# Optimization experiments

Hardware: AMD Instinct MI355X
Metric: run time of the kernel (lower is better)

## Reference

```python
import jax, jax.numpy as jnp
import numpy as np

NEG = -1e30  # finite stand-in for -inf so softmax grads stay clean


def setup_inputs() -> dict:
    key = jax.random.key(0)
    k1, k2 = jax.random.split(key)
    C, D = 8192, 512
    gt_class_embeddings = jax.random.normal(k1, (C, D), dtype=jnp.float32)
    w = jax.random.normal(k2, (C, D), dtype=jnp.float32)
    return {"gt_class_embeddings": gt_class_embeddings, "w": w}


def reference(gt_class_embeddings, w):
    # L2-normalize class embeddings, cosine-similarity matrix S (diag == 1)
    G = gt_class_embeddings / jnp.linalg.norm(gt_class_embeddings, axis=-1, keepdims=True)
    S = G @ G.T  # [C, C]
    C = S.shape[0]
    off_diag = ~jnp.eye(C, dtype=bool)

    # seSoftmax: per-row softmax over entries != 1 (off-diagonal); diagonal stays 1
    P = jax.nn.softmax(jnp.where(off_diag, S, NEG), axis=-1)
    S2 = jnp.where(off_diag, P, 1.0)

    # argsort(-S2)[1] == most similar (diag value 1 always ranks first),
    # argsort(-S2)[-1] == least similar == row min (softmax values < 1)
    ms = jnp.argmax(jnp.where(off_diag, S2, NEG), axis=-1)  # [C]
    ls = jnp.argmin(jnp.where(off_diag, S2, -NEG), axis=-1)  # [C]

    rows = jnp.arange(C)
    margin = S2[rows, ms] - S2[rows, ls]  # [C]

    d_ms = jnp.sqrt(jnp.sum((w - w[ms]) ** 2, axis=-1))  # [C]
    d_ls = jnp.sqrt(jnp.sum((w - w[ls]) ** 2, axis=-1))  # [C]

    loss = jnp.mean(jnp.maximum(0.0, d_ms - d_ls + margin))
    return loss
```

## Files before the change

### kernel.cpp

```cpp
#include <hip/hip_runtime.h>
#include <math.h>

#define CDIM 8192
#define DDIM 512
#define NEGF -3.0e38f
#define POSF  3.0e38f

#define NSLOT 64

typedef __attribute__((ext_vector_type(8))) short bf16x8;
typedef __attribute__((ext_vector_type(4))) float f32x4;

__device__ __forceinline__ unsigned short f2bf(float x) {
    unsigned int u = __float_as_uint(x);
    u += 0x7fffu + ((u >> 16) & 1u);
    return (unsigned short)(u >> 16);
}
__device__ __forceinline__ float bf2f(unsigned short h) {
    return __uint_as_float(((unsigned int)h) << 16);
}
__device__ __forceinline__ void gld16(const void* g, void* l) {
    __builtin_amdgcn_global_load_lds(
        (__attribute__((address_space(1))) void*)(void*)g,
        (__attribute__((address_space(3))) void*)l, 16, 0, 0);
}

__global__ __launch_bounds__(256) void k_prep(const float* __restrict__ g,
                                              unsigned short* __restrict__ hi,
                                              unsigned short* __restrict__ lo) {
    const int wave = threadIdx.x >> 6;
    const int lane = threadIdx.x & 63;
    const int row = blockIdx.x * 4 + wave;
    const float4* src = (const float4*)(g + (size_t)row * DDIM);
    const float4 a = src[lane * 2];
    const float4 b = src[lane * 2 + 1];
    float s = a.x * a.x + a.y * a.y + a.z * a.z + a.w * a.w +
              b.x * b.x + b.y * b.y + b.z * b.z + b.w * b.w;
#pragma unroll
    for (int m = 1; m < 64; m <<= 1) s += __shfl_xor(s, m, 64);
    const float rn = rsqrtf(s);
    const float y[8] = {a.x * rn, a.y * rn, a.z * rn, a.w * rn,
                        b.x * rn, b.y * rn, b.z * rn, b.w * rn};
    unsigned int hv[4], lv[4];
#pragma unroll
    for (int i = 0; i < 4; ++i) {
        const unsigned short h0 = f2bf(y[2 * i]);
        const unsigned short h1 = f2bf(y[2 * i + 1]);
        const unsigned short l0 = f2bf(y[2 * i] - bf2f(h0));
        const unsigned short l1 = f2bf(y[2 * i + 1] - bf2f(h1));
        hv[i] = (unsigned int)h0 | ((unsigned int)h1 << 16);
        lv[i] = (unsigned int)l0 | ((unsigned int)l1 << 16);
    }
    uint4* dh = (uint4*)(hi + (size_t)row * DDIM + lane * 8);
    uint4* dl = (uint4*)(lo + (size_t)row * DDIM + lane * 8);
    *dh = make_uint4(hv[0], hv[1], hv[2], hv[3]);
    *dl = make_uint4(lv[0], lv[1], lv[2], lv[3]);
}

__global__ __launch_bounds__(512, 2) void k_simstats(
    const unsigned short* __restrict__ ghi, const unsigned short* __restrict__ glo,
    float* __restrict__ pmax, float* __restrict__ pmin, float* __restrict__ pZ,
    int* __restrict__ pamax, int* __restrict__ pamin) {
    const int bid = blockIdx.x;
    const int e = (bid & 7) * 132 + (bid >> 3);
    int J = 0, base = 0;
    while (true) {
        const int cnt = (J >> 1) + 1;
        if (e < base + cnt) break;
        base += cnt; ++J;
    }
    const int I = e - base;
    const bool typeD0 = (J == 2 * I);
    const bool typeD1 = (J == 2 * I + 1);

    __shared__ unsigned short SH[3 * 24576];
    const int t = threadIdx.x;
    const int wave = t >> 6;
    const int lane = t & 63;
    const int lanelo = lane & 15;
    const int quad = lane >> 4;
    const int wr = wave >> 1;
    const int wc = wave & 1;

    const int srow = t >> 2;
    const int scolb = ((t & 3) ^ ((t >> 3) & 3)) << 4;

    const int fsl = (quad ^ ((lanelo >> 1) & 3)) << 3;
    const int aoff = (wr * 64 + lanelo) * 32 + fsl;
    const int boff = (wc * 64 + lanelo) * 32 + fsl;

    float* rm  = (float*)SH;
    float* rmn = rm + 512;
    float* rz  = rmn + 512;
    int*   ra  = (int*)(rz + 512);
    int*   ran = ra + 512;
    float* cm  = (float*)(ran + 512);
    float* cmn = cm + 512;
    float* cz  = cmn + 512;
    int*   ca  = (int*)(cz + 512);
    int*   can = ca + 512;

    const int i0 = I * 256;
    const int j0 = J * 128;

    f32x4 acc[4][4];
#pragma unroll
    for (int rt = 0; rt < 4; ++rt)
#pragma unroll
        for (int ct = 0; ct < 4; ++ct)
            acc[rt][ct] = (f32x4){0.f, 0.f, 0.f, 0.f};

    const char* baseAh = (const char*)ghi + (size_t)(i0 + srow) * 1024 + scolb;
    const char* baseAl = (const char*)glo + (size_t)(i0 + srow) * 1024 + scolb;
    const char* baseBh = (const char*)ghi + (size_t)(j0 + srow) * 1024 + scolb;
    const char* baseBl = (const char*)glo + (size_t)(j0 + srow) * 1024 + scolb;

    auto STG_A = [&](int ks, int b, int half) {
        char* d = (char*)SH + b * 49152 + half * 16384 + t * 16;
        const char* gb = half ? baseAl : baseAh;
        const size_t cb = (size_t)ks * 64;
        gld16(gb + cb, d);
        gld16(gb + 131072 + cb, d + 8192);
    };
    auto STG_B = [&](int ks, int b, int half) {
        char* d = (char*)SH + b * 49152 + 32768 + half * 8192 + t * 16;
        const char* gb = half ? baseBl : baseBh;
        gld16(gb + (size_t)ks * 64, d);
    };

    STG_A(0, 0, 0); STG_A(0, 0, 1); STG_B(0, 0, 0); STG_B(0, 0, 1);
    STG_A(1, 1, 0); STG_A(1, 1, 1); STG_B(1, 1, 0); STG_B(1, 1, 1);
    asm volatile("s_waitcnt vmcnt(6)" ::: "memory");
    __builtin_amdgcn_s_barrier();
    asm volatile("" ::: "memory");

#pragma unroll
    for (int ks = 0; ks < 16; ++ks) {
        const unsigned short* buf = SH + (ks % 3) * 24576;
        const int sb = (ks + 2) % 3;
        const bool st = (ks <= 13);
        bf16x8 ah[4], bh[4];
        {
            if (st) STG_A(ks + 2, sb, 0);
            bf16x8 bl[4];
#pragma unroll
            for (int rt = 0; rt < 4; ++rt)
                ah[rt] = *(const bf16x8*)&buf[aoff + rt * 512];
#pragma unroll
            for (int ct = 0; ct < 4; ++ct)
                bl[ct] = *(const bf16x8*)&buf[20480 + boff + ct * 512];
            asm volatile("" ::: "memory");
            __builtin_amdgcn_s_barrier();
            asm volatile("s_waitcnt lgkmcnt(0)" ::: "memory");
            __builtin_amdgcn_s_setprio(1);
#pragma unroll
            for (int ct = 0; ct < 4; ++ct)
#pragma unroll
                for (int rt = 0; rt < 4; ++rt)
                    acc[rt][ct] = __builtin_amdgcn_mfma_f32_16x16x32_bf16(
                        ah[rt], bl[ct], acc[rt][ct], 0, 0, 0);
            __builtin_amdgcn_s_setprio(0);
            asm volatile("" ::: "memory");
            __builtin_amdgcn_s_barrier();
            asm volatile("" ::: "memory");
        }
        {
            if (st) STG_A(ks + 2, sb, 1);
#pragma unroll
            for (int ct = 0; ct < 4; ++ct)
                bh[ct] = *(const bf16x8*)&buf[16384 + boff + ct * 512];
            asm volatile("" ::: "memory");
            __builtin_amdgcn_s_barrier();
            asm volatile("s_waitcnt lgkmcnt(0)" ::: "memory");
            __builtin_amdgcn_s_setprio(1);
#pragma unroll
            for (int ct = 0; ct < 4; ++ct)
#pragma unroll
                for (int rt = 0; rt < 4; ++rt)
                    acc[rt][ct] = __builtin_amdgcn_mfma_f32_16x16x32_bf16(
                        ah[rt], bh[ct], acc[rt][ct], 0, 0, 0);
            __builtin_amdgcn_s_setprio(0);
            asm volatile("" ::: "memory");
            __builtin_amdgcn_s_barrier();
            asm volatile("" ::: "memory");
        }
        {
            if (st) { STG_B(ks + 2, sb, 0); STG_B(ks + 2, sb, 1); }
            bf16x8 al[4];
#pragma unroll
            for (int rt = 0; rt < 4; ++rt)
                al[rt] = *(const bf16x8*)&buf[8192 + aoff + rt * 512];
            if (ks <= 13) asm volatile("s_waitcnt vmcnt(6)" ::: "memory");
            else if (ks == 14) asm volatile("s_waitcnt vmcnt(0)" ::: "memory");
            asm volatile("" ::: "memory");
            __builtin_amdgcn_s_barrier();
            asm volatile("s_waitcnt lgkmcnt(0)" ::: "memory");
            __builtin_amdgcn_s_setprio(1);
#pragma unroll
            for (int ct = 0; ct < 4; ++ct)
#pragma unroll
                for (int rt = 0; rt < 4; ++rt)
                    acc[rt][ct] = __builtin_amdgcn_mfma_f32_16x16x32_bf16(
                        al[rt], bh[ct], acc[rt][ct], 0, 0, 0);
            __builtin_amdgcn_s_setprio(0);
            asm volatile("" ::: "memory");
            __builtin_amdgcn_s_barrier();
            asm volatile("" ::: "memory");
        }
    }

    const bool mask_d = (typeD0 && wr < 2) || (typeD1 && wr >= 2);

#pragma unroll
    for (int rt = 0; rt < 4; ++rt) {
#pragma unroll
        for (int r = 0; r < 4; ++r) {
            const int lrow = wr * 64 + rt * 16 + quad * 4 + r;
            const int gi = i0 + lrow;
            float tmax = NEGF; int targ = 0;
            float tmin = POSF; int targn = 0;
#pragma unroll
            for (int ct = 0; ct < 4; ++ct) {
                const int gj = j0 + wc * 64 + ct * 16 + lanelo;
                const float v = acc[rt][ct][r];
                const bool dg = mask_d && (gj == gi);
                const float vM = dg ? NEGF : v;
                const float vm = dg ? POSF : v;
                if (vM > tmax) { tmax = vM; targ = gj; }
                if (vm < tmin) { tmin = vm; targn = gj; }
            }
#pragma unroll
            for (int msk = 1; msk < 16; msk <<= 1) {
                const float v2 = __shfl_xor(tmax, msk, 64);
                const int i2 = __shfl_xor(targ, msk, 64);
                if (v2 > tmax) { tmax = v2; targ = i2; }
                const float v3 = __shfl_xor(tmin, msk, 64);
                const int i3 = __shfl_xor(targn, msk, 64);
                if (v3 < tmin) { tmin = v3; targn = i3; }
            }
            if (lanelo == 0) {
                const int o = wc * 256 + lrow;
                rm[o] = tmax; rmn[o] = tmin;
                ra[o] = targ; ran[o] = targn;
            }
        }
    }

    const bool col_ok = (!typeD0 && !typeD1) || (typeD1 && wr < 2);
    if (col_ok) {
#pragma unroll
        for (int ct = 0; ct < 4; ++ct) {
            const int lcol = wc * 64 + ct * 16 + lanelo;
            float tmax = NEGF; int targ = 0;
            float tmin = POSF; int targn = 0;
#pragma unroll
            for (int rt = 0; rt < 4; ++rt)
#pragma unroll
                for (int r = 0; r < 4; ++r) {
                    const int gi = i0 + wr * 64 + rt * 16 + quad * 4 + r;
                    const float v = acc[rt][ct][r];
                    if (v > tmax) { tmax = v; targ = gi; }
                    if (v < tmin) { tmin = v; targn = gi; }
                }
#pragma unroll
            for (int msk = 16; msk < 64; msk <<= 1) {
                const float m2v = __shfl_xor(tmax, msk, 64);
                const int i2 = __shfl_xor(targ, msk, 64);
                if (m2v > tmax) { tmax = m2v; targ = i2; }
                const float mn2 = __shfl_xor(tmin, msk, 64);
                const int in2 = __shfl_xor(targn, msk, 64);
                if (mn2 < tmin) { tmin = mn2; targn = in2; }
            }
            if (quad == 0) {
                const int o = wr * 128 + lcol;
                cm[o] = tmax; cmn[o] = tmin;
                ca[o] = targ; can[o] = targn;
            }
        }
    }

#pragma unroll
    for (int rt = 0; rt < 4; ++rt)
#pragma unroll
        for (int ct = 0; ct < 4; ++ct)
#pragma unroll
            for (int r = 0; r < 4; ++r)
                acc[rt][ct][r] = __expf(acc[rt][ct][r] - 1.f);
    if ((typeD0 && wr < 2 && wr == wc) ||
        (typeD1 && wr >= 2 && (wr - 2) == wc)) {
#pragma unroll
        for (int rt = 0; rt < 4; ++rt)
#pragma unroll
            for (int r = 0; r < 4; ++r)
                if (lanelo == quad * 4 + r) acc[rt][rt][r] = 0.f;
    }

#pragma unroll
    for (int rt = 0; rt < 4; ++rt)
#pragma unroll
        for (int r = 0; r < 4; ++r) {
            float s = acc[rt][0][r] + acc[rt][1][r] +
                      acc[rt][2][r] + acc[rt][3][r];
#pragma unroll
            for (int msk = 1; msk < 16; msk <<= 1) s += __shfl_xor(s, msk, 64);
            if (lanelo == 0)
                rz[wc * 256 + wr * 64 + rt * 16 + quad * 4 + r] = s;
        }

    if (col_ok) {
#pragma unroll
        for (int ct = 0; ct < 4; ++ct) {
            float s = 0.f;
#pragma unroll
            for (int rt = 0; rt < 4; ++rt)
                s += acc[rt][ct][0] + acc[rt][ct][1] +
                     acc[rt][ct][2] + acc[rt][ct][3];
#pragma unroll
            for (int msk = 16; msk < 64; msk <<= 1) s += __shfl_xor(s, msk, 64);
            if (quad == 0)
                cz[wr * 128 + wc * 64 + ct * 16 + lanelo] = s;
        }
    }

    __syncthreads();

    if (t < 256) {
        if (!(typeD0 && t >= 128)) {
            const float m0 = rm[t], m1 = rm[256 + t];
            float vmax = m0; int imax = ra[t];
            if (m1 > vmax) { vmax = m1; imax = ra[256 + t]; }
            float vmin = rmn[t]; int imin = ran[t];
            if (rmn[256 + t] < vmin) { vmin = rmn[256 + t]; imin = ran[256 + t]; }
            const size_t o = (size_t)J * CDIM + i0 + t;
            pmax[o] = vmax; pmin[o] = vmin; pZ[o] = rz[t] + rz[256 + t];
            pamax[o] = imax; pamin[o] = imin;
        }
    } else {
        const int tt = t - 256;
        const int h = tt >> 7;
        const int col = tt & 127;
        const bool ok = (!typeD0 && !typeD1) || (typeD1 && h == 0);
        if (ok) {
            const int b0 = h * 256 + col, b1 = h * 256 + 128 + col;
            const float m0 = cm[b0], m1 = cm[b1];
            float vmax = m0; int imax = ca[b0];
            if (m1 > vmax) { vmax = m1; imax = ca[b1]; }
            float vmin = cmn[b0]; int imin = can[b0];
            if (cmn[b1] < vmin) { vmin = cmn[b1]; imin = can[b1]; }
            const size_t o = (size_t)(2 * I + h) * CDIM + j0 + col;
            pmax[o] = vmax; pmin[o] = vmin; pZ[o] = cz[b0] + cz[b1];
            pamax[o] = imax; pamin[o] = imin;
        }
    }
}

__global__ __launch_bounds__(256) void k_lossc(
    const float* __restrict__ pmax, const float* __restrict__ pmin,
    const float* __restrict__ pZ, const int* __restrict__ pamax,
    const int* __restrict__ pamin, const float* __restrict__ w,
    float* __restrict__ vals) {
    const int wave = threadIdx.x >> 6;
    const int lane = threadIdx.x & 63;
    const int row = blockIdx.x * 4 + wave;
    const size_t o = (size_t)lane * CDIM + row;
    float v = pmax[o]; int a = pamax[o];
    float u = pmin[o]; int b = pamin[o];
    float z = pZ[o];
#pragma unroll
    for (int msk = 1; msk < 64; msk <<= 1) {
        const float v2 = __shfl_xor(v, msk, 64);
        const int i2 = __shfl_xor(a, msk, 64);
        if (v2 > v) { v = v2; a = i2; }
        const float v3 = __shfl_xor(u, msk, 64);
        const int i3 = __shfl_xor(b, msk, 64);
        if (v3 < u) { u = v3; b = i3; }
        z += __shfl_xor(z, msk, 64);
    }
    const float margin = (1.f - __expf(u - v)) * __expf(v - 1.f) / z;
    const int jm = a, jl = b;

    const float4* wi = (const float4*)(w + (size_t)row * DDIM);
    const float4* wm = (const float4*)(w + (size_t)jm * DDIM);
    const float4* wl = (const float4*)(w + (size_t)jl * DDIM);
    float sm = 0.f, sl = 0.f;
#pragma unroll
    for (int h = 0; h < 2; ++h) {
        const int idx = h * 64 + lane;
        const float4 x = wi[idx];
        const float4 y = wm[idx];
        const float4 c = wl[idx];
        float d;
        d = x.x - y.x; sm = fmaf(d, d, sm);
        d = x.y - y.y; sm = fmaf(d, d, sm);
        d = x.z - y.z; sm = fmaf(d, d, sm);
        d = x.w - y.w; sm = fmaf(d, d, sm);
        d = x.x - c.x; sl = fmaf(d, d, sl);
        d = x.y - c.y; sl = fmaf(d, d, sl);
        d = x.z - c.z; sl = fmaf(d, d, sl);
        d = x.w - c.w; sl = fmaf(d, d, sl);
    }
#pragma unroll
    for (int msk = 1; msk < 64; msk <<= 1) {
        sm += __shfl_xor(sm, msk, 64);
        sl += __shfl_xor(sl, msk, 64);
    }
    if (lane == 0) {
        const float val = sqrtf(sm) - sqrtf(sl) + margin;
        vals[row] = val > 0.f ? val : 0.f;
    }
}

__global__ __launch_bounds__(256) void k_final(const float* __restrict__ vals,
                                               float* __restrict__ out) {
    __shared__ float red[256];
    float s = 0.f;
    for (int i = threadIdx.x; i < CDIM; i += 256) s += vals[i];
    red[threadIdx.x] = s;
    __syncthreads();
#pragma unroll
    for (int k = 128; k > 0; k >>= 1) {
        if (threadIdx.x < (unsigned)k) red[threadIdx.x] += red[threadIdx.x + k];
        __syncthreads();
    }
    if (threadIdx.x == 0) out[0] = red[0] * (1.0f / CDIM);
}

extern "C" void kernel_launch(void* const* d_in, const int* in_sizes, int n_in,
                              void* d_out, int out_size, void* d_ws, size_t ws_size,
                              hipStream_t stream) {
    const float* g = (const float*)d_in[0];
    const float* w = (const float*)d_in[1];
    float* out = (float*)d_out;

    unsigned short* ghi = (unsigned short*)d_ws;
    unsigned short* glo = ghi + (size_t)CDIM * DDIM;
    float* p = (float*)(glo + (size_t)CDIM * DDIM);
    float* pmax = p;      p += (size_t)NSLOT * CDIM;
    float* pmin = p;      p += (size_t)NSLOT * CDIM;
    float* pZ = p;        p += (size_t)NSLOT * CDIM;
    int* pamax = (int*)p; p += (size_t)NSLOT * CDIM;
    int* pamin = (int*)p; p += (size_t)NSLOT * CDIM;
    float* vals = p;      p += CDIM;

    k_prep<<<CDIM / 4, 256, 0, stream>>>(g, ghi, glo);
    k_simstats<<<1056, 512, 0, stream>>>(ghi, glo, pmax, pmin, pZ, pamax, pamin);
    k_lossc<<<CDIM / 4, 256, 0, stream>>>(pmax, pmin, pZ, pamax, pamin, w, vals);
    k_final<<<1, 256, 0, stream>>>(vals, out);
}
```

Before: 270.6 us.

## Remap triangular tiles to XCD-local supertiles and simplify K-loop pipeline

```diff
diff --git a/kernel.cpp b/kernel.cpp
--- a/kernel.cpp
+++ b/kernel.cpp
@@ -57,19 +57,40 @@
     *dl = make_uint4(lv[0], lv[1], lv[2], lv[3]);
 }
 
+__device__ __constant__ unsigned char OSUPX[16] = {
+    1, 2, 10, 3,   11, 19, 4, 12,   20, 28, 5, 13,   21, 29, 37, 6};
+__device__ __constant__ unsigned char OSUPY[12] = {
+    14, 22, 30,   38, 46, 7,   15, 23, 31,   39, 47, 55};
+
 __global__ __launch_bounds__(512, 2) void k_simstats(
     const unsigned short* __restrict__ ghi, const unsigned short* __restrict__ glo,
     float* __restrict__ pmax, float* __restrict__ pmin, float* __restrict__ pZ,
     int* __restrict__ pamax, int* __restrict__ pamin) {
     const int bid = blockIdx.x;
-    const int e = (bid & 7) * 132 + (bid >> 3);
-    int J = 0, base = 0;
-    while (true) {
-        const int cnt = (J >> 1) + 1;
-        if (e < base + cnt) break;
-        base += cnt; ++J;
-    }
-    const int I = e - base;
+    const int xcd = bid & 7;
+    const int off = bid >> 3;
+    int I, J;
+    if (xcd < 4) {
+        if (off >= 128) return;
+        const int code = OSUPX[xcd * 4 + (off >> 5)];
+        const int u = off & 31;
+        I = (code >> 3) * 4 + (u & 3);
+        J = (code & 7) * 8 + (u >> 2);
+    } else if (off < 96) {
+        const int code = OSUPY[(xcd - 4) * 3 + (off >> 5)];
+        const int u = off & 31;
+        I = (code >> 3) * 4 + (u & 3);
+        J = (code & 7) * 8 + (u >> 2);
+    } else {
+        const int d = off - 96;
+        const int s = (xcd - 4) + ((d >= 20) ? 4 : 0);
+        int u = (d >= 20) ? d - 20 : d;
+        int jj = 0, pre = 0;
+        while (true) { const int c = (jj >> 1) + 1;
+                       if (u < pre + c) break; pre += c; ++jj; }
+        I = s * 4 + (u - pre);
+        J = s * 8 + jj;
+    }
     const bool typeD0 = (J == 2 * I);
     const bool typeD1 = (J == 2 * I + 1);
 
@@ -132,81 +153,47 @@
     STG_A(1, 1, 0); STG_A(1, 1, 1); STG_B(1, 1, 0); STG_B(1, 1, 1);
     asm volatile("s_waitcnt vmcnt(6)" ::: "memory");
     __builtin_amdgcn_s_barrier();
-    asm volatile("" ::: "memory");
 
 #pragma unroll
     for (int ks = 0; ks < 16; ++ks) {
         const unsigned short* buf = SH + (ks % 3) * 24576;
         const int sb = (ks + 2) % 3;
-        const bool st = (ks <= 13);
-        bf16x8 ah[4], bh[4];
-        {
-            if (st) STG_A(ks + 2, sb, 0);
-            bf16x8 bl[4];
+        if (ks <= 13) {
+            STG_A(ks + 2, sb, 0); STG_A(ks + 2, sb, 1);
+            STG_B(ks + 2, sb, 0); STG_B(ks + 2, sb, 1);
+        }
+        bf16x8 ah[4], al[4], bh[4], bl[4];
+#pragma unroll
+        for (int rt = 0; rt < 4; ++rt) {
+            ah[rt] = *(const bf16x8*)&buf[aoff + rt * 512];
+            al[rt] = *(const bf16x8*)&buf[8192 + aoff + rt * 512];
+        }
+#pragma unroll
+        for (int ct = 0; ct < 4; ++ct) {
+            bh[ct] = *(const bf16x8*)&buf[16384 + boff + ct * 512];
+            bl[ct] = *(const bf16x8*)&buf[20480 + boff + ct * 512];
+        }
+#pragma unroll
+        for (int ct = 0; ct < 4; ++ct)
 #pragma unroll
             for (int rt = 0; rt < 4; ++rt)
-                ah[rt] = *(const bf16x8*)&buf[aoff + rt * 512];
-#pragma unroll
-            for (int ct = 0; ct < 4; ++ct)
-                bl[ct] = *(const bf16x8*)&buf[20480 + boff + ct * 512];
-            asm volatile("" ::: "memory");
-            __builtin_amdgcn_s_barrier();
-            asm volatile("s_waitcnt lgkmcnt(0)" ::: "memory");
-            __builtin_amdgcn_s_setprio(1);
-#pragma unroll
-            for (int ct = 0; ct < 4; ++ct)
-#pragma unroll
-                for (int rt = 0; rt < 4; ++rt)
-                    acc[rt][ct] = __builtin_amdgcn_mfma_f32_16x16x32_bf16(
-                        ah[rt], bl[ct], acc[rt][ct], 0, 0, 0);
-            __builtin_amdgcn_s_setprio(0);
-            asm volatile("" ::: "memory");
-            __builtin_amdgcn_s_barrier();
-            asm volatile("" ::: "memory");
-        }
-        {
-            if (st) STG_A(ks + 2, sb, 1);
-#pragma unroll
-            for (int ct = 0; ct < 4; ++ct)
-                bh[ct] = *(const bf16x8*)&buf[16384 + boff + ct * 512];
-            asm volatile("" ::: "memory");
-            __builtin_amdgcn_s_barrier();
-            asm volatile("s_waitcnt lgkmcnt(0)" ::: "memory");
-            __builtin_amdgcn_s_setprio(1);
-#pragma unroll
-            for (int ct = 0; ct < 4; ++ct)
-#pragma unroll
-                for (int rt = 0; rt < 4; ++rt)
-                    acc[rt][ct] = __builtin_amdgcn_mfma_f32_16x16x32_bf16(
-                        ah[rt], bh[ct], acc[rt][ct], 0, 0, 0);
-            __builtin_amdgcn_s_setprio(0);
-            asm volatile("" ::: "memory");
-            __builtin_amdgcn_s_barrier();
-            asm volatile("" ::: "memory");
-        }
-        {
-            if (st) { STG_B(ks + 2, sb, 0); STG_B(ks + 2, sb, 1); }
-            bf16x8 al[4];
+                acc[rt][ct] = __builtin_amdgcn_mfma_f32_16x16x32_bf16(
+                    ah[rt], bl[ct], acc[rt][ct], 0, 0, 0);
+#pragma unroll
+        for (int ct = 0; ct < 4; ++ct)
 #pragma unroll
             for (int rt = 0; rt < 4; ++rt)
-                al[rt] = *(const bf16x8*)&buf[8192 + aoff + rt * 512];
-            if (ks <= 13) asm volatile("s_waitcnt vmcnt(6)" ::: "memory");
-            else if (ks == 14) asm volatile("s_waitcnt vmcnt(0)" ::: "memory");
-            asm volatile("" ::: "memory");
-            __builtin_amdgcn_s_barrier();
-            asm volatile("s_waitcnt lgkmcnt(0)" ::: "memory");
-            __builtin_amdgcn_s_setprio(1);
-#pragma unroll
-            for (int ct = 0; ct < 4; ++ct)
-#pragma unroll
-                for (int rt = 0; rt < 4; ++rt)
-                    acc[rt][ct] = __builtin_amdgcn_mfma_f32_16x16x32_bf16(
-                        al[rt], bh[ct], acc[rt][ct], 0, 0, 0);
-            __builtin_amdgcn_s_setprio(0);
-            asm volatile("" ::: "memory");
-            __builtin_amdgcn_s_barrier();
-            asm volatile("" ::: "memory");
-        }
+                acc[rt][ct] = __builtin_amdgcn_mfma_f32_16x16x32_bf16(
+                    ah[rt], bh[ct], acc[rt][ct], 0, 0, 0);
+#pragma unroll
+        for (int ct = 0; ct < 4; ++ct)
+#pragma unroll
+            for (int rt = 0; rt < 4; ++rt)
+                acc[rt][ct] = __builtin_amdgcn_mfma_f32_16x16x32_bf16(
+                    al[rt], bh[ct], acc[rt][ct], 0, 0, 0);
+        if (ks <= 13)      asm volatile("s_waitcnt vmcnt(6)" ::: "memory");
+        else if (ks == 14) asm volatile("s_waitcnt vmcnt(0)" ::: "memory");
+        __builtin_amdgcn_s_barrier();
     }
 
     const bool mask_d = (typeD0 && wr < 2) || (typeD1 && wr >= 2);
@@ -443,7 +430,7 @@
     float* vals = p;      p += CDIM;
 
     k_prep<<<CDIM / 4, 256, 0, stream>>>(g, ghi, glo);
-    k_simstats<<<1056, 512, 0, stream>>>(ghi, glo, pmax, pmin, pZ, pamax, pamin);
+    k_simstats<<<1088, 512, 0, stream>>>(ghi, glo, pmax, pmin, pZ, pamax, pamin);
     k_lossc<<<CDIM / 4, 256, 0, stream>>>(pmax, pmin, pZ, pamax, pamin, w, vals);
     k_final<<<1, 256, 0, stream>>>(vals, out);
 }
```

New measurement: 263.1 us. 2.7% less time.
